# Optimization experiments

Hardware: AMD Instinct MI355X
Metric: run time of the kernel (lower is better)

Reference implementation:

```python
import jax, jax.numpy as jnp
import numpy as np

SMOOTHING_VAR = 0.1  # self.smoothing_var in the torch module

def setup_inputs() -> dict:
    key = jax.random.key(0)
    inputs = jax.random.normal(key, (32, 2048, 512), dtype=jnp.float32)  # [B, T, D]
    return {"inputs": inputs}

def reference(inputs) -> jnp.ndarray:
    # Eval-mode path of SpikingActivation.forward (second definition):
    #   smoothing = sigmoid(0.1 * inputs[:, 1])          [B, D]
    #   level_0 = 1; level_t = (1-s)*x_t + s*level_{t-1}
    #   return stack of levels along time dim            [B, T, D]
    s = jax.nn.sigmoid(SMOOTHING_VAR * inputs[:, 1])  # [B, D]
    one_minus_s = 1.0 - s
    level0 = jnp.ones_like(s)  # scalar 1 broadcast to [B, D]

    def step(level, x_t):
        level = one_minus_s * x_t + s * level
        return level, level

    xs = jnp.swapaxes(inputs, 0, 1)  # [T, B, D]
    _, levels = jax.lax.scan(step, level0, xs)  # [T, B, D]
    return jnp.swapaxes(levels, 0, 1)  # [B, T, D]
```

## Files before the change

### kernel.cpp

```cpp
#include <hip/hip_runtime.h>
#include <math.h>

#define B 32
#define T 2048
#define D 512
#define D4 (D / 4)

#define CHUNK 32
#define WARM 32

__global__ __launch_bounds__(D4) void spiking_scan_kernel(
    const float4* __restrict__ x, float4* __restrict__ out) {
    const int d4    = threadIdx.x;
    const int chunk = blockIdx.x;
    const int b     = blockIdx.y;

    const float4 xs = x[((size_t)b * T + 1) * D4 + d4];
    float s[4], oms[4], level[4];
    s[0] = 1.0f / (1.0f + __expf(-0.1f * xs.x));
    s[1] = 1.0f / (1.0f + __expf(-0.1f * xs.y));
    s[2] = 1.0f / (1.0f + __expf(-0.1f * xs.z));
    s[3] = 1.0f / (1.0f + __expf(-0.1f * xs.w));
    #pragma unroll
    for (int c = 0; c < 4; ++c) { oms[c] = 1.0f - s[c]; level[c] = 1.0f; }

    const int t0    = chunk * CHUNK;
    const int tw    = (chunk == 0) ? 0 : (t0 - WARM);
    const int nwarm = t0 - tw;

    const float4* xp = x + ((size_t)b * T + tw) * D4 + d4;

    for (int t = 0; t < nwarm; t += 8) {
        float4 v[8];
        #pragma unroll
        for (int j = 0; j < 8; ++j) v[j] = xp[(size_t)j * D4];
        #pragma unroll
        for (int j = 0; j < 8; ++j) {
            level[0] = fmaf(oms[0], v[j].x, s[0] * level[0]);
            level[1] = fmaf(oms[1], v[j].y, s[1] * level[1]);
            level[2] = fmaf(oms[2], v[j].z, s[2] * level[2]);
            level[3] = fmaf(oms[3], v[j].w, s[3] * level[3]);
        }
        xp += (size_t)8 * D4;
    }

    float4* op = out + ((size_t)b * T + t0) * D4 + d4;
    for (int t = 0; t < CHUNK; t += 8) {
        float4 v[8];
        #pragma unroll
        for (int j = 0; j < 8; ++j) v[j] = xp[(size_t)j * D4];
        #pragma unroll
        for (int j = 0; j < 8; ++j) {
            level[0] = fmaf(oms[0], v[j].x, s[0] * level[0]);
            level[1] = fmaf(oms[1], v[j].y, s[1] * level[1]);
            level[2] = fmaf(oms[2], v[j].z, s[2] * level[2]);
            level[3] = fmaf(oms[3], v[j].w, s[3] * level[3]);
            float4 o; o.x = level[0]; o.y = level[1]; o.z = level[2]; o.w = level[3];
            op[(size_t)j * D4] = o;
        }
        xp += (size_t)8 * D4;
        op += (size_t)8 * D4;
    }
}

extern "C" void kernel_launch(void* const* d_in, const int* in_sizes, int n_in,
                              void* d_out, int out_size, void* d_ws, size_t ws_size,
                              hipStream_t stream) {
    const float4* x = (const float4*)d_in[0];
    float4* out     = (float4*)d_out;
    dim3 grid(T / CHUNK, B);
    dim3 block(D4);
    spiking_scan_kernel<<<grid, block, 0, stream>>>(x, out);
}
```

Before: 251.0 us.

## Software-pipeline chunk loads with double buffering and pack two chunks per block

Rewrites the chunked scan so each thread prefetches the next eight timesteps into registers while computing on the current eight. The warm-up and output phases are fully unrolled into one pipelined loop. Blocks now hold two chunks (2D block of 128x2 threads) with launch bounds of 256 threads and 4 blocks, which halves the grid and is meant to hide global memory latency. The cost is higher register pressure from the double buffer, which could limit occupancy.

```diff
diff --git a/kernel.cpp b/kernel.cpp
--- a/kernel.cpp
+++ b/kernel.cpp
@@ -9,10 +9,10 @@
 #define CHUNK 32
 #define WARM 32
 
-__global__ __launch_bounds__(D4) void spiking_scan_kernel(
+__global__ __launch_bounds__(256, 4) void spiking_scan_kernel(
     const float4* __restrict__ x, float4* __restrict__ out) {
     const int d4    = threadIdx.x;
-    const int chunk = blockIdx.x;
+    const int chunk = blockIdx.x * 2 + threadIdx.y;
     const int b     = blockIdx.y;
 
     const float4 xs = x[((size_t)b * T + 1) * D4 + d4];
@@ -24,42 +24,77 @@
     #pragma unroll
     for (int c = 0; c < 4; ++c) { oms[c] = 1.0f - s[c]; level[c] = 1.0f; }
 
-    const int t0    = chunk * CHUNK;
-    const int tw    = (chunk == 0) ? 0 : (t0 - WARM);
-    const int nwarm = t0 - tw;
+    const int t0 = chunk * CHUNK;
+    float4* op = out + ((size_t)b * T + t0) * D4 + d4;
 
-    const float4* xp = x + ((size_t)b * T + tw) * D4 + d4;
-
-    for (int t = 0; t < nwarm; t += 8) {
-        float4 v[8];
+    if (chunk == 0) {
+        const float4* xp = x + ((size_t)b * T) * D4 + d4;
+        float4 cur[8];
         #pragma unroll
-        for (int j = 0; j < 8; ++j) v[j] = xp[(size_t)j * D4];
+        for (int j = 0; j < 8; ++j) cur[j] = xp[(size_t)j * D4];
+        xp += (size_t)8 * D4;
         #pragma unroll
-        for (int j = 0; j < 8; ++j) {
-            level[0] = fmaf(oms[0], v[j].x, s[0] * level[0]);
-            level[1] = fmaf(oms[1], v[j].y, s[1] * level[1]);
-            level[2] = fmaf(oms[2], v[j].z, s[2] * level[2]);
-            level[3] = fmaf(oms[3], v[j].w, s[3] * level[3]);
+        for (int i = 0; i < 4; ++i) {
+            float4 nxt[8];
+            if (i < 3) {
+                #pragma unroll
+                for (int j = 0; j < 8; ++j) nxt[j] = xp[(size_t)j * D4];
+                xp += (size_t)8 * D4;
+            }
+            #pragma unroll
+            for (int j = 0; j < 8; ++j) {
+                level[0] = fmaf(oms[0], cur[j].x, s[0] * level[0]);
+                level[1] = fmaf(oms[1], cur[j].y, s[1] * level[1]);
+                level[2] = fmaf(oms[2], cur[j].z, s[2] * level[2]);
+                level[3] = fmaf(oms[3], cur[j].w, s[3] * level[3]);
+                float4 o; o.x = level[0]; o.y = level[1]; o.z = level[2]; o.w = level[3];
+                op[(size_t)j * D4] = o;
+            }
+            op += (size_t)8 * D4;
+            if (i < 3) {
+                #pragma unroll
+                for (int j = 0; j < 8; ++j) cur[j] = nxt[j];
+            }
         }
+    } else {
+        const float4* xp = x + ((size_t)b * T + t0 - WARM) * D4 + d4;
+        float4 cur[8];
+        #pragma unroll
+        for (int j = 0; j < 8; ++j) cur[j] = xp[(size_t)j * D4];
         xp += (size_t)8 * D4;
-    }
-
-    float4* op = out + ((size_t)b * T + t0) * D4 + d4;
-    for (int t = 0; t < CHUNK; t += 8) {
-        float4 v[8];
         #pragma unroll
-        for (int j = 0; j < 8; ++j) v[j] = xp[(size_t)j * D4];
-        #pragma unroll
-        for (int j = 0; j < 8; ++j) {
-            level[0] = fmaf(oms[0], v[j].x, s[0] * level[0]);
-            level[1] = fmaf(oms[1], v[j].y, s[1] * level[1]);
-            level[2] = fmaf(oms[2], v[j].z, s[2] * level[2]);
-            level[3] = fmaf(oms[3], v[j].w, s[3] * level[3]);
-            float4 o; o.x = level[0]; o.y = level[1]; o.z = level[2]; o.w = level[3];
-            op[(size_t)j * D4] = o;
+        for (int i = 0; i < 8; ++i) {
+            float4 nxt[8];
+            if (i < 7) {
+                #pragma unroll
+                for (int j = 0; j < 8; ++j) nxt[j] = xp[(size_t)j * D4];
+                xp += (size_t)8 * D4;
+            }
+            if (i < 4) {
+                #pragma unroll
+                for (int j = 0; j < 8; ++j) {
+                    level[0] = fmaf(oms[0], cur[j].x, s[0] * level[0]);
+                    level[1] = fmaf(oms[1], cur[j].y, s[1] * level[1]);
+                    level[2] = fmaf(oms[2], cur[j].z, s[2] * level[2]);
+                    level[3] = fmaf(oms[3], cur[j].w, s[3] * level[3]);
+                }
+            } else {
+                #pragma unroll
+                for (int j = 0; j < 8; ++j) {
+                    level[0] = fmaf(oms[0], cur[j].x, s[0] * level[0]);
+                    level[1] = fmaf(oms[1], cur[j].y, s[1] * level[1]);
+                    level[2] = fmaf(oms[2], cur[j].z, s[2] * level[2]);
+                    level[3] = fmaf(oms[3], cur[j].w, s[3] * level[3]);
+                    float4 o; o.x = level[0]; o.y = level[1]; o.z = level[2]; o.w = level[3];
+                    op[(size_t)j * D4] = o;
+                }
+                op += (size_t)8 * D4;
+            }
+            if (i < 7) {
+                #pragma unroll
+                for (int j = 0; j < 8; ++j) cur[j] = nxt[j];
+            }
         }
-        xp += (size_t)8 * D4;
-        op += (size_t)8 * D4;
     }
 }
 
@@ -68,7 +103,7 @@
                               hipStream_t stream) {
     const float4* x = (const float4*)d_in[0];
     float4* out     = (float4*)d_out;
-    dim3 grid(T / CHUNK, B);
-    dim3 block(D4);
+    dim3 grid(T / CHUNK / 2, B);
+    dim3 block(D4, 2);
     spiking_scan_kernel<<<grid, block, 0, stream>>>(x, out);
 }
```

New measurement: 241.3 us. -3.9%, faster.
